# Kernel tuning notes

Hardware: AMD Instinct MI355X
Metric: run time of the kernel (lower is better)

Reference implementation:

```python
import jax, jax.numpy as jnp
import numpy as np

TEMPERATURE = 0.5   # cfg.LOSS.TEMPERATURE
REG = 0.5           # Sinkhorn entropic regularization
NUM_ITER = 100      # numItermax in forward call
STOP_THR = 1e-9

BS, NUM_CLASSES, DIM = 16384, 1000, 512


def _l2norm(x):
    return x / jnp.linalg.norm(x, axis=-1, keepdims=True)


def setup_inputs() -> dict:
    key = jax.random.key(0)
    k1, k2, k3 = jax.random.split(key, 3)
    features = _l2norm(jax.random.normal(k1, (BS, DIM), jnp.float32))
    text_features = _l2norm(jax.random.normal(k2, (NUM_CLASSES, DIM), jnp.float32))
    ratios = jax.random.uniform(k3, (NUM_CLASSES,), jnp.float32)
    ratios = ratios / ratios.sum()  # class prior, sums to 1
    return {"features": features, "text_features": text_features, "ratios": ratios}


def sinkhorn_knopp(a, b, M, reg):
    """Faithful Sinkhorn-Knopp: u/v scaling loop with NaN/Inf bail-out and
    every-10-iters convergence check, unrolled as a masked lax.scan."""
    dim_a, dim_b = a.shape[0], b.shape[0]
    K = jnp.exp(M / -reg)                 # [dim_a, dim_b]
    Kp = (1.0 / a)[:, None] * K           # [dim_a, dim_b]
    u0 = jnp.ones((dim_a,), M.dtype) / dim_a
    v0 = jnp.ones((dim_b,), M.dtype) / dim_b

    def step(carry, ii):
        u, v, done = carry
        KtU = K.T @ u                     # [dim_b]
        v_new = b / KtU
        u_new = 1.0 / (Kp @ v_new)        # [dim_a]
        bad = (jnp.any(KtU == 0)
               | jnp.any(~jnp.isfinite(u_new))
               | jnp.any(~jnp.isfinite(v_new)))
        # err check (original does it when ii % 10 == 0)
        tmp2 = (u_new @ K) * v_new        # einsum('i,ij,j->j', u, K, v)
        err = jnp.linalg.norm(tmp2 - b)
        converged = ((ii % 10) == 0) & (err < STOP_THR)
        keep_prev = done | bad            # revert to uprev/vprev on bad, freeze after done
        u2 = jnp.where(keep_prev, u, u_new)
        v2 = jnp.where(keep_prev, v, v_new)
        return (u2, v2, done | bad | converged), None

    (u, v, _), _ = jax.lax.scan(step, (u0, v0, jnp.array(False)), jnp.arange(NUM_ITER))
    return u[:, None] * K * v[None, :]


def reference(features, text_features, ratios):
    sim_matrix = (features @ text_features.T) / TEMPERATURE   # [bs, C]
    cost_matrix = 1.0 - sim_matrix
    bs = features.shape[0]
    a = jnp.ones((bs,), features.dtype)       # row marginal (uniform over batch)
    b = ratios * bs                            # column marginal (class ratios)
    plan = sinkhorn_knopp(a, b, sim_matrix / cost_matrix, REG)  # [bs, C]
    return plan
```

## Files before the change

### kernel.cpp

```cpp
#include <hip/hip_runtime.h>
#include <hip/hip_bf16.h>

typedef float   f32x4_t  __attribute__((ext_vector_type(4)));
typedef float   f32x2_t  __attribute__((ext_vector_type(2)));
typedef __bf16  bf16x8_t __attribute__((ext_vector_type(8)));
typedef int     i32x4_t  __attribute__((ext_vector_type(4)));

#define N_ROWS   16384
#define N_COLS   1000
#define N_COLS_P 1024
#define N_DIM    512
#define N_ITER   100
#define PBLK     256
#define PTHR     512
#define NRED     64

__device__ __forceinline__ int ldi_sc1(const int* p) {
    return __hip_atomic_load(p, __ATOMIC_RELAXED, __HIP_MEMORY_SCOPE_AGENT);
}
__device__ __forceinline__ void addi_sc1(int* p) {
    __hip_atomic_fetch_add(p, 1, __ATOMIC_RELAXED, __HIP_MEMORY_SCOPE_AGENT);
}
__device__ __forceinline__ f32x2_t ld2_coh(const float* p) {
    f32x2_t v;
    asm volatile("global_load_dwordx2 %0, %1, off sc0 sc1\n\t"
                 "s_waitcnt vmcnt(0)"
                 : "=&v"(v) : "v"(p) : "memory");
    return v;
}
__device__ __forceinline__ void ld4x2_coh(const float* pA, const float* pB,
                                          f32x4_t* a, f32x4_t* b) {
    asm volatile("global_load_dwordx4 %0, %2, off sc0 sc1\n\t"
                 "global_load_dwordx4 %1, %3, off sc0 sc1\n\t"
                 "s_waitcnt vmcnt(0)"
                 : "=&v"(*a), "=&v"(*b) : "v"(pA), "v"(pB) : "memory");
}
__device__ __forceinline__ void st2_coh(float* p, f32x2_t v) {
    asm volatile("global_store_dwordx2 %0, %1, off sc0 sc1"
                 :: "v"(p), "v"(v) : "memory");
}
__device__ __forceinline__ void st1_coh(float* p, float v) {
    asm volatile("global_store_dword %0, %1, off sc0 sc1"
                 :: "v"(p), "v"(v) : "memory");
}
__device__ __forceinline__ void drain_vmem() {
    asm volatile("s_waitcnt vmcnt(0)" ::: "memory");
}

__device__ __forceinline__ unsigned short f2bf(float f) {
    unsigned int u = __builtin_bit_cast(unsigned int, f);
    u += 0x7FFFu + ((u >> 16) & 1u);
    return (unsigned short)(u >> 16);
}

template <int MODE>
__launch_bounds__(256)
__global__ void k_gemm(const float* __restrict__ F, const float* __restrict__ T,
                       void* __restrict__ Kout, float* __restrict__ cpart,
                       const float* __restrict__ v_com, const float* __restrict__ u_both,
                       const int* __restrict__ flags)
{
    __shared__ unsigned short lA[128 * 72];
    __shared__ unsigned short lB[128 * 72];
    __shared__ float cs_lds[4 * 64];

    const int bm = blockIdx.x;
    const int bn = blockIdx.y;
    const int m0 = bm << 7;
    const int n0 = bn << 7;
    const int t  = threadIdx.x;
    const int lane = t & 63;
    const int wid  = t >> 6;
    const int wr = wid >> 1;
    const int wc = wid & 1;

    f32x4_t acc[4][4];
#pragma unroll
    for (int a = 0; a < 4; ++a)
#pragma unroll
        for (int b = 0; b < 4; ++b)
            acc[a][b] = (f32x4_t){0.f, 0.f, 0.f, 0.f};

    const int srow = t >> 4;
    const int scol = (t & 15) << 2;

    for (int kt = 0; kt < N_DIM; kt += 64) {
#pragma unroll
        for (int r = 0; r < 8; ++r) {
            const int rr = srow + (r << 4);
            const float4 av = *(const float4*)(F + (size_t)(m0 + rr) * N_DIM + kt + scol);
            ushort4 a4; a4.x = f2bf(av.x); a4.y = f2bf(av.y); a4.z = f2bf(av.z); a4.w = f2bf(av.w);
            *(ushort4*)(&lA[rr * 72 + scol]) = a4;
            const int gn = n0 + rr;
            float4 bv = make_float4(0.f, 0.f, 0.f, 0.f);
            if (gn < N_COLS) bv = *(const float4*)(T + (size_t)gn * N_DIM + kt + scol);
            ushort4 b4; b4.x = f2bf(bv.x); b4.y = f2bf(bv.y); b4.z = f2bf(bv.z); b4.w = f2bf(bv.w);
            *(ushort4*)(&lB[rr * 72 + scol]) = b4;
        }
        __syncthreads();
#pragma unroll
        for (int ks = 0; ks < 2; ++ks) {
            bf16x8_t afr[4], bfr[4];
#pragma unroll
            for (int mf = 0; mf < 4; ++mf) {
                const int r = (wr << 6) + (mf << 4) + (lane & 15);
                const int off = r * 72 + (ks << 5) + ((lane >> 4) << 3);
                afr[mf] = __builtin_bit_cast(bf16x8_t, *(const i32x4_t*)(&lA[off]));
            }
#pragma unroll
            for (int nf = 0; nf < 4; ++nf) {
                const int r = (wc << 6) + (nf << 4) + (lane & 15);
                const int off = r * 72 + (ks << 5) + ((lane >> 4) << 3);
                bfr[nf] = __builtin_bit_cast(bf16x8_t, *(const i32x4_t*)(&lB[off]));
            }
#pragma unroll
            for (int mf = 0; mf < 4; ++mf)
#pragma unroll
                for (int nf = 0; nf < 4; ++nf)
                    acc[mf][nf] = __builtin_amdgcn_mfma_f32_16x16x32_bf16(
                        afr[mf], bfr[nf], acc[mf][nf], 0, 0, 0);
        }
        __syncthreads();
    }

    int usel = 2;
    if (MODE == 1) usel = flags[1];
    float csum[4] = {0.f, 0.f, 0.f, 0.f};
#pragma unroll
    for (int mf = 0; mf < 4; ++mf) {
#pragma unroll
        for (int nf = 0; nf < 4; ++nf) {
#pragma unroll
            for (int j = 0; j < 4; ++j) {
                const float d = acc[mf][nf][j];
                const float s = 2.f * d;
                const float M = s / (1.f - s);
                const float kv = __expf(-2.f * M);
                const int grow = m0 + (wr << 6) + (mf << 4) + ((lane >> 4) << 2) + j;
                const int gcol = n0 + (wc << 6) + (nf << 4) + (lane & 15);
                if (MODE == 0) {
                    ((unsigned short*)Kout)[(size_t)grow * N_COLS_P + gcol] =
                        (gcol < N_COLS) ? f2bf(kv) : (unsigned short)0;
                    csum[nf] += kv;
                } else {
                    if (gcol < N_COLS) {
                        const float u = (usel == 2) ? (1.f / 16384.f)
                                                    : u_both[(size_t)usel * N_ROWS + grow];
                        ((float*)Kout)[(size_t)grow * N_COLS + gcol] = u * kv * v_com[gcol];
                    }
                }
            }
        }
    }
    if (MODE == 0) {
#pragma unroll
        for (int nf = 0; nf < 4; ++nf) {
            csum[nf] += __shfl_xor(csum[nf], 16);
            csum[nf] += __shfl_xor(csum[nf], 32);
        }
        if (lane < 16) {
#pragma unroll
            for (int nf = 0; nf < 4; ++nf)
                cs_lds[wid * 64 + (nf << 4) + lane] = csum[nf];
        }
        __syncthreads();
        if (t < 128) {
            const int cw = t >> 6;
            const int c6 = t & 63;
            cpart[(size_t)bm * N_COLS_P + n0 + t] =
                cs_lds[cw * 64 + c6] + cs_lds[(cw + 2) * 64 + c6];
        }
    }
}

__launch_bounds__(128)
__global__ void k_init(const float* __restrict__ cpart, float* __restrict__ ktu0,
                       float* __restrict__ vcom, int* __restrict__ flags,
                       int* __restrict__ pcnt, int* __restrict__ rcnt,
                       int* __restrict__ flags2)
{
    const int j = blockIdx.x * 128 + threadIdx.x;
    if (j < N_COLS) {
        float s = 0.f;
        for (int p = 0; p < 128; ++p) s += cpart[(size_t)p * N_COLS_P + j];
        ktu0[j] = s * (1.f / 16384.f);
        vcom[j] = 1.f / 1000.f;
    } else {
        ktu0[j] = 1.f;
        vcom[j] = 0.f;
    }
    for (int z = j; z < 2048; z += 1024) { pcnt[z] = 0; rcnt[z] = 0; flags2[z] = 0; }
    if (j < 4) flags[j] = (j == 1) ? 2 : 0;
}

__launch_bounds__(PTHR, 2)
__global__ void k_persist(const unsigned short* __restrict__ Kb,
                          const float* __restrict__ ratios,
                          float* __restrict__ ktu,
                          float* __restrict__ utmp,
                          float* __restrict__ vcom,
                          float* __restrict__ partials,
                          int* __restrict__ flags,
                          int* __restrict__ pcnt,
                          int* __restrict__ rcnt,
                          int* __restrict__ flags2)
{
    __shared__ float vbuf[2][N_COLS_P];
    __shared__ float wp[8][N_COLS_P];
    __shared__ float redw[8][16];
    __shared__ float rbc;
    __shared__ int ibc;
    const int t = threadIdx.x, lane = t & 63, wid = t >> 6, b = blockIdx.x;
    const int row0 = (b << 6) + (wid << 3);
    const int c2 = t << 1;
    const bool isred = (b < NRED);

    unsigned kp[8][8];
#pragma unroll
    for (int r = 0; r < 8; ++r) {
        const unsigned* rp = (const unsigned*)(Kb + (size_t)(row0 + r) * N_COLS_P);
#pragma unroll
        for (int q = 0; q < 8; ++q) kp[r][q] = rp[(q << 6) + lane];
    }
    const float bj0 = (c2 < N_COLS) ? ratios[c2] * 16384.f : 0.f;
    const float bj1 = (c2 + 1 < N_COLS) ? ratios[c2 + 1] * 16384.f : 0.f;

    int usel = 2;

    for (int ii = 0; ii <= N_ITER; ++ii) {
        const int p = ii & 1;
        f32x2_t kc;

        if (ii > 0) {
            if (t == 0) {
                while (ldi_sc1(&rcnt[(ii - 1) << 4]) < NRED)
                    __builtin_amdgcn_s_sleep(1);
                ibc = ldi_sc1(&flags2[(ii - 1) << 4]);
            }
            __syncthreads();
            if (ibc) break;
            usel = (ii - 1) & 1;
            kc = ld2_coh(&ktu[(p << 10) + c2]);
            if (((ii - 1) % 10) == 0) {
                const float vo0 = vbuf[usel][c2], vo1 = vbuf[usel][c2 + 1];
                const float d0 = (c2 < N_COLS) ? kc[0] * vo0 - bj0 : 0.f;
                const float d1 = (c2 + 1 < N_COLS) ? kc[1] * vo1 - bj1 : 0.f;
                float e = d0 * d0 + d1 * d1;
#pragma unroll
                for (int sh = 1; sh <= 32; sh <<= 1) e += __shfl_xor(e, sh);
                if (lane == 0) redw[wid][0] = e;
                __syncthreads();
                if (t == 0) {
                    float s = 0.f;
#pragma unroll
                    for (int w = 0; w < 8; ++w) s += redw[w][0];
                    rbc = s;
                }
                __syncthreads();
                if (rbc < 1e-18f) break;
            }
            if (ii == N_ITER) break;
        } else {
            kc = ld2_coh(&ktu[c2]);
        }

        const float v0 = bj0 / kc[0];
        const float v1 = bj1 / kc[1];
        const int badv = (kc[0] == 0.f) | (kc[1] == 0.f) |
                         (!isfinite(v0)) | (!isfinite(v1));
        *(f32x2_t*)&vbuf[p][c2] = (f32x2_t){v0, v1};
        if (__syncthreads_or(badv)) break;

        float vr[16];
#pragma unroll
        for (int q = 0; q < 8; ++q) {
            const f32x2_t vv = *(const f32x2_t*)&vbuf[p][(q << 7) + (lane << 1)];
            vr[2*q] = vv[0]; vr[2*q+1] = vv[1];
        }
        float dots[8];
#pragma unroll
        for (int r = 0; r < 8; ++r) {
            float p0 = 0.f, p1 = 0.f, p2 = 0.f, p3 = 0.f;
#pragma unroll
            for (int q = 0; q < 8; ++q) {
                const unsigned u = kp[r][q];
                const float lo = __builtin_bit_cast(float, u << 16);
                const float hi = __builtin_bit_cast(float, u & 0xFFFF0000u);
                if (q & 1) { p2 = fmaf(lo, vr[2*q], p2); p3 = fmaf(hi, vr[2*q+1], p3); }
                else       { p0 = fmaf(lo, vr[2*q], p0); p1 = fmaf(hi, vr[2*q+1], p1); }
            }
            dots[r] = (p0 + p1) + (p2 + p3);
        }
#pragma unroll
        for (int s = 1; s <= 32; s <<= 1) {
#pragma unroll
            for (int r = 0; r < 8; ++r) dots[r] += __shfl_xor(dots[r], s);
        }
        float u8[8];
        int ubad = 0;
#pragma unroll
        for (int r = 0; r < 8; ++r) { u8[r] = 1.f / dots[r]; ubad |= !isfinite(u8[r]); }
        if (lane == 0) {
            float* uo = utmp + ((size_t)p << 14) + row0;
#pragma unroll
            for (int r = 0; r < 8; ++r) uo[r] = u8[r];
        }
        if (__any(ubad) && lane == 0)
            __hip_atomic_fetch_or(&flags2[ii << 4], 1, __ATOMIC_RELAXED,
                                  __HIP_MEMORY_SCOPE_AGENT);

        float creg[16];
#pragma unroll
        for (int e = 0; e < 16; ++e) creg[e] = 0.f;
#pragma unroll
        for (int r = 0; r < 8; ++r) {
#pragma unroll
            for (int q = 0; q < 8; ++q) {
                const unsigned u = kp[r][q];
                const float lo = __builtin_bit_cast(float, u << 16);
                const float hi = __builtin_bit_cast(float, u & 0xFFFF0000u);
                creg[2*q]   = fmaf(lo, u8[r], creg[2*q]);
                creg[2*q+1] = fmaf(hi, u8[r], creg[2*q+1]);
            }
        }
#pragma unroll
        for (int q = 0; q < 8; ++q)
            *(f32x2_t*)&wp[wid][(q << 7) + (lane << 1)] = (f32x2_t){creg[2*q], creg[2*q+1]};
        __syncthreads();
        {
            const int j2 = t << 1;
            f32x2_t s2 = *(const f32x2_t*)&wp[0][j2];
#pragma unroll
            for (int w = 1; w < 8; ++w) {
                const f32x2_t x = *(const f32x2_t*)&wp[w][j2];
                s2[0] += x[0]; s2[1] += x[1];
            }
            st2_coh(&partials[((size_t)b << 10) + j2], s2);
        }
        drain_vmem();
        __syncthreads();
        if (t == 0) addi_sc1(&pcnt[ii << 4]);

        if (isred) {
            if (t == 0) {
                while (ldi_sc1(&pcnt[ii << 4]) < PBLK)
                    __builtin_amdgcn_s_sleep(1);
            }
            __syncthreads();
            const int cbase = (b << 4) + ((lane & 3) << 2);
            const int rowA  = (wid << 4) + (lane >> 2);
            f32x4_t a, bq;
            ld4x2_coh(&partials[((size_t)rowA << 10) + cbase],
                      &partials[((size_t)(rowA + 128) << 10) + cbase], &a, &bq);
            f32x4_t s4;
#pragma unroll
            for (int e = 0; e < 4; ++e) s4[e] = a[e] + bq[e];
#pragma unroll
            for (int sh = 4; sh <= 32; sh <<= 1) {
#pragma unroll
                for (int e = 0; e < 4; ++e) s4[e] += __shfl_xor(s4[e], sh);
            }
            if (lane < 4) *(f32x4_t*)&redw[wid][lane << 2] = s4;
            __syncthreads();
            if (t < 16) {
                float s2 = 0.f;
#pragma unroll
                for (int w = 0; w < 8; ++w) s2 += redw[w][t];
                const int c = (b << 4) + t;
                st1_coh(&ktu[(((ii + 1) & 1) << 10) + c], (c < N_COLS) ? s2 : 1.f);
            }
            drain_vmem();
            __syncthreads();
            if (t == 0) addi_sc1(&rcnt[ii << 4]);
        }
    }

    if (b == 0) {
        if (c2 < N_COLS)
            vcom[c2] = (usel == 2) ? (1.f / 1000.f) : vbuf[usel][c2];
        if (c2 + 1 < N_COLS)
            vcom[c2 + 1] = (usel == 2) ? (1.f / 1000.f) : vbuf[usel][c2 + 1];
        if (t == 0) flags[1] = usel;
    }
}

extern "C" void kernel_launch(void* const* d_in, const int* in_sizes, int n_in,
                              void* d_out, int out_size, void* d_ws, size_t ws_size,
                              hipStream_t stream)
{
    const float* F      = (const float*)d_in[0];
    const float* T      = (const float*)d_in[1];
    const float* ratios = (const float*)d_in[2];
    float* out = (float*)d_out;
    unsigned short* Kb = (unsigned short*)d_out;

    float* ws        = (float*)d_ws;
    float* partials  = ws;
    float* ktu       = partials + (size_t)PBLK * N_COLS_P;
    float* utmp      = ktu + 2 * N_COLS_P;
    float* vcom      = utmp + 2 * N_ROWS;
    int*   flags     = (int*)(vcom + N_COLS_P);
    int*   pcnt      = flags + 16;
    int*   rcnt      = pcnt + 2048;
    int*   flags2    = rcnt + 2048;
    const size_t need_bytes = ((size_t)PBLK * N_COLS_P + 2 * N_COLS_P + 2 * N_ROWS +
                               N_COLS_P) * sizeof(float) +
                              (16 + 3 * 2048) * sizeof(int);
    if (ws_size < need_bytes) return;

    k_gemm<0><<<dim3(128, 8), 256, 0, stream>>>(F, T, Kb, partials, nullptr, nullptr, flags);
    k_init<<<8, 128, 0, stream>>>(partials, ktu, vcom, flags, pcnt, rcnt, flags2);
    k_persist<<<PBLK, PTHR, 0, stream>>>(Kb, ratios, ktu, utmp, vcom, partials,
                                         flags, pcnt, rcnt, flags2);
    k_gemm<1><<<dim3(128, 8), 256, 0, stream>>>(F, T, out, nullptr, vcom, utmp, flags);
}
```

Baseline: 2.235 ms.

## Replace two-phase partial reduction with float atomics into per-iteration slots

Each block now atomically adds its per-column partial sums into a per-iteration slot buffer, padded to 16 bytes per column. This removes the dedicated reducer blocks and leaves one global barrier per iteration instead of two, so the write-partials / wait / reduce / wait chain collapses into one atomic accumulation and one counter wait. In exchange it issues 256×1000 float atomics per iteration, which contend on the same addresses, and it adds an init kernel that zeroes 100 slots. It also drops the per-row u non-finite check and only detects bad values through non-finite column sums, and the atomics make the summation order nondeterministic.

```diff
diff --git a/kernel.cpp b/kernel.cpp
--- a/kernel.cpp
+++ b/kernel.cpp
@@ -13,7 +13,7 @@
 #define N_ITER   100
 #define PBLK     256
 #define PTHR     512
-#define NRED     64
+#define SLOTF    4096
 
 __device__ __forceinline__ int ldi_sc1(const int* p) {
     return __hip_atomic_load(p, __ATOMIC_RELAXED, __HIP_MEMORY_SCOPE_AGENT);
@@ -21,27 +21,15 @@
 __device__ __forceinline__ void addi_sc1(int* p) {
     __hip_atomic_fetch_add(p, 1, __ATOMIC_RELAXED, __HIP_MEMORY_SCOPE_AGENT);
 }
-__device__ __forceinline__ f32x2_t ld2_coh(const float* p) {
-    f32x2_t v;
-    asm volatile("global_load_dwordx2 %0, %1, off sc0 sc1\n\t"
+__device__ __forceinline__ void addf_sc1(float* p, float v) {
+    __hip_atomic_fetch_add(p, v, __ATOMIC_RELAXED, __HIP_MEMORY_SCOPE_AGENT);
+}
+__device__ __forceinline__ void ld2x1_coh(const float* p0, const float* p1,
+                                          float* a, float* b) {
+    asm volatile("global_load_dword %0, %2, off sc0 sc1\n\t"
+                 "global_load_dword %1, %3, off sc0 sc1\n\t"
                  "s_waitcnt vmcnt(0)"
-                 : "=&v"(v) : "v"(p) : "memory");
-    return v;
-}
-__device__ __forceinline__ void ld4x2_coh(const float* pA, const float* pB,
-                                          f32x4_t* a, f32x4_t* b) {
-    asm volatile("global_load_dwordx4 %0, %2, off sc0 sc1\n\t"
-                 "global_load_dwordx4 %1, %3, off sc0 sc1\n\t"
-                 "s_waitcnt vmcnt(0)"
-                 : "=&v"(*a), "=&v"(*b) : "v"(pA), "v"(pB) : "memory");
-}
-__device__ __forceinline__ void st2_coh(float* p, f32x2_t v) {
-    asm volatile("global_store_dwordx2 %0, %1, off sc0 sc1"
-                 :: "v"(p), "v"(v) : "memory");
-}
-__device__ __forceinline__ void st1_coh(float* p, float v) {
-    asm volatile("global_store_dword %0, %1, off sc0 sc1"
-                 :: "v"(p), "v"(v) : "memory");
+                 : "=&v"(*a), "=&v"(*b) : "v"(p0), "v"(p1) : "memory");
 }
 __device__ __forceinline__ void drain_vmem() {
     asm volatile("s_waitcnt vmcnt(0)" ::: "memory");
@@ -174,46 +162,51 @@
 }
 
 __launch_bounds__(128)
-__global__ void k_init(const float* __restrict__ cpart, float* __restrict__ ktu0,
-                       float* __restrict__ vcom, int* __restrict__ flags,
-                       int* __restrict__ pcnt, int* __restrict__ rcnt,
-                       int* __restrict__ flags2)
+__global__ void k_init1(const float* __restrict__ cpart, float* __restrict__ ktu0)
 {
     const int j = blockIdx.x * 128 + threadIdx.x;
     if (j < N_COLS) {
         float s = 0.f;
         for (int p = 0; p < 128; ++p) s += cpart[(size_t)p * N_COLS_P + j];
         ktu0[j] = s * (1.f / 16384.f);
-        vcom[j] = 1.f / 1000.f;
     } else {
         ktu0[j] = 1.f;
-        vcom[j] = 0.f;
-    }
-    for (int z = j; z < 2048; z += 1024) { pcnt[z] = 0; rcnt[z] = 0; flags2[z] = 0; }
-    if (j < 4) flags[j] = (j == 1) ? 2 : 0;
+    }
+}
+
+__launch_bounds__(256)
+__global__ void k_init2(float* __restrict__ slots, int* __restrict__ done,
+                        int* __restrict__ flags)
+{
+    const int idx = blockIdx.x * 256 + threadIdx.x;
+    if (idx < N_ITER * 1024) {
+        f32x4_t v = (f32x4_t){0.f, 0.f, 0.f, 0.f};
+        if ((idx & 1023) >= N_COLS) v[0] = 1.f;
+        *(f32x4_t*)&slots[(size_t)idx << 2] = v;
+    }
+    if (blockIdx.x == 0) {
+        for (int z = threadIdx.x; z < N_ITER * 16; z += 256) done[z] = 0;
+        if (threadIdx.x < 16) flags[threadIdx.x] = (threadIdx.x == 1) ? 2 : 0;
+    }
 }
 
 __launch_bounds__(PTHR, 2)
 __global__ void k_persist(const unsigned short* __restrict__ Kb,
                           const float* __restrict__ ratios,
-                          float* __restrict__ ktu,
+                          const float* __restrict__ ktu0,
+                          float* __restrict__ slots,
                           float* __restrict__ utmp,
                           float* __restrict__ vcom,
-                          float* __restrict__ partials,
                           int* __restrict__ flags,
-                          int* __restrict__ pcnt,
-                          int* __restrict__ rcnt,
-                          int* __restrict__ flags2)
+                          int* __restrict__ done)
 {
     __shared__ float vbuf[2][N_COLS_P];
     __shared__ float wp[8][N_COLS_P];
-    __shared__ float redw[8][16];
+    __shared__ float cw[8];
     __shared__ float rbc;
-    __shared__ int ibc;
     const int t = threadIdx.x, lane = t & 63, wid = t >> 6, b = blockIdx.x;
     const int row0 = (b << 6) + (wid << 3);
     const int c2 = t << 1;
-    const bool isred = (b < NRED);
 
     unsigned kp[8][8];
 #pragma unroll
@@ -228,32 +221,33 @@
     int usel = 2;
 
     for (int ii = 0; ii <= N_ITER; ++ii) {
-        const int p = ii & 1;
-        f32x2_t kc;
+        const int sp = ii & 1;
+        float kc0, kc1;
 
         if (ii > 0) {
             if (t == 0) {
-                while (ldi_sc1(&rcnt[(ii - 1) << 4]) < NRED)
+                while (ldi_sc1(&done[(ii - 1) << 4]) < PBLK)
                     __builtin_amdgcn_s_sleep(1);
-                ibc = ldi_sc1(&flags2[(ii - 1) << 4]);
             }
             __syncthreads();
-            if (ibc) break;
+            const float* sl = slots + (size_t)(ii - 1) * SLOTF;
+            ld2x1_coh(sl + (size_t)c2 * 4, sl + (size_t)c2 * 4 + 4, &kc0, &kc1);
+            const int badk = (!isfinite(kc0)) | (!isfinite(kc1));
+            if (__syncthreads_or(badk)) break;
             usel = (ii - 1) & 1;
-            kc = ld2_coh(&ktu[(p << 10) + c2]);
             if (((ii - 1) % 10) == 0) {
                 const float vo0 = vbuf[usel][c2], vo1 = vbuf[usel][c2 + 1];
-                const float d0 = (c2 < N_COLS) ? kc[0] * vo0 - bj0 : 0.f;
-                const float d1 = (c2 + 1 < N_COLS) ? kc[1] * vo1 - bj1 : 0.f;
+                const float d0 = (c2 < N_COLS) ? kc0 * vo0 - bj0 : 0.f;
+                const float d1 = (c2 + 1 < N_COLS) ? kc1 * vo1 - bj1 : 0.f;
                 float e = d0 * d0 + d1 * d1;
 #pragma unroll
                 for (int sh = 1; sh <= 32; sh <<= 1) e += __shfl_xor(e, sh);
-                if (lane == 0) redw[wid][0] = e;
+                if (lane == 0) cw[wid] = e;
                 __syncthreads();
                 if (t == 0) {
                     float s = 0.f;
 #pragma unroll
-                    for (int w = 0; w < 8; ++w) s += redw[w][0];
+                    for (int w = 0; w < 8; ++w) s += cw[w];
                     rbc = s;
                 }
                 __syncthreads();
@@ -261,20 +255,21 @@
             }
             if (ii == N_ITER) break;
         } else {
-            kc = ld2_coh(&ktu[c2]);
-        }
-
-        const float v0 = bj0 / kc[0];
-        const float v1 = bj1 / kc[1];
-        const int badv = (kc[0] == 0.f) | (kc[1] == 0.f) |
+            kc0 = ktu0[c2];
+            kc1 = ktu0[c2 + 1];
+        }
+
+        const float v0 = bj0 / kc0;
+        const float v1 = bj1 / kc1;
+        const int badv = (kc0 == 0.f) | (kc1 == 0.f) |
                          (!isfinite(v0)) | (!isfinite(v1));
-        *(f32x2_t*)&vbuf[p][c2] = (f32x2_t){v0, v1};
+        vbuf[sp][c2] = v0; vbuf[sp][c2 + 1] = v1;
         if (__syncthreads_or(badv)) break;
 
         float vr[16];
 #pragma unroll
         for (int q = 0; q < 8; ++q) {
-            const f32x2_t vv = *(const f32x2_t*)&vbuf[p][(q << 7) + (lane << 1)];
+            const f32x2_t vv = *(const f32x2_t*)&vbuf[sp][(q << 7) + (lane << 1)];
             vr[2*q] = vv[0]; vr[2*q+1] = vv[1];
         }
         float dots[8];
@@ -297,17 +292,13 @@
             for (int r = 0; r < 8; ++r) dots[r] += __shfl_xor(dots[r], s);
         }
         float u8[8];
-        int ubad = 0;
-#pragma unroll
-        for (int r = 0; r < 8; ++r) { u8[r] = 1.f / dots[r]; ubad |= !isfinite(u8[r]); }
+#pragma unroll
+        for (int r = 0; r < 8; ++r) u8[r] = 1.f / dots[r];
         if (lane == 0) {
-            float* uo = utmp + ((size_t)p << 14) + row0;
+            float* uo = utmp + ((size_t)sp << 14) + row0;
 #pragma unroll
             for (int r = 0; r < 8; ++r) uo[r] = u8[r];
         }
-        if (__any(ubad) && lane == 0)
-            __hip_atomic_fetch_or(&flags2[ii << 4], 1, __ATOMIC_RELAXED,
-                                  __HIP_MEMORY_SCOPE_AGENT);
 
         float creg[16];
 #pragma unroll
@@ -335,44 +326,13 @@
                 const f32x2_t x = *(const f32x2_t*)&wp[w][j2];
                 s2[0] += x[0]; s2[1] += x[1];
             }
-            st2_coh(&partials[((size_t)b << 10) + j2], s2);
+            float* sl = slots + (size_t)ii * SLOTF;
+            if (j2 < N_COLS)     addf_sc1(sl + (size_t)j2 * 4, s2[0]);
+            if (j2 + 1 < N_COLS) addf_sc1(sl + (size_t)(j2 + 1) * 4, s2[1]);
         }
         drain_vmem();
         __syncthreads();
-        if (t == 0) addi_sc1(&pcnt[ii << 4]);
-
-        if (isred) {
-            if (t == 0) {
-                while (ldi_sc1(&pcnt[ii << 4]) < PBLK)
-                    __builtin_amdgcn_s_sleep(1);
-            }
-            __syncthreads();
-            const int cbase = (b << 4) + ((lane & 3) << 2);
-            const int rowA  = (wid << 4) + (lane >> 2);
-            f32x4_t a, bq;
-            ld4x2_coh(&partials[((size_t)rowA << 10) + cbase],
-                      &partials[((size_t)(rowA + 128) << 10) + cbase], &a, &bq);
-            f32x4_t s4;
-#pragma unroll
-            for (int e = 0; e < 4; ++e) s4[e] = a[e] + bq[e];
-#pragma unroll
-            for (int sh = 4; sh <= 32; sh <<= 1) {
-#pragma unroll
-                for (int e = 0; e < 4; ++e) s4[e] += __shfl_xor(s4[e], sh);
-            }
-            if (lane < 4) *(f32x4_t*)&redw[wid][lane << 2] = s4;
-            __syncthreads();
-            if (t < 16) {
-                float s2 = 0.f;
-#pragma unroll
-                for (int w = 0; w < 8; ++w) s2 += redw[w][t];
-                const int c = (b << 4) + t;
-                st1_coh(&ktu[(((ii + 1) & 1) << 10) + c], (c < N_COLS) ? s2 : 1.f);
-            }
-            drain_vmem();
-            __syncthreads();
-            if (t == 0) addi_sc1(&rcnt[ii << 4]);
-        }
+        if (t == 0) addi_sc1(&done[ii << 4]);
     }
 
     if (b == 0) {
@@ -395,22 +355,22 @@
     unsigned short* Kb = (unsigned short*)d_out;
 
     float* ws        = (float*)d_ws;
-    float* partials  = ws;
-    float* ktu       = partials + (size_t)PBLK * N_COLS_P;
-    float* utmp      = ktu + 2 * N_COLS_P;
+    float* slots     = ws;
+    float* cpart     = slots;
+    float* ktu0      = slots + (size_t)N_ITER * SLOTF;
+    float* utmp      = ktu0 + N_COLS_P;
     float* vcom      = utmp + 2 * N_ROWS;
     int*   flags     = (int*)(vcom + N_COLS_P);
-    int*   pcnt      = flags + 16;
-    int*   rcnt      = pcnt + 2048;
-    int*   flags2    = rcnt + 2048;
-    const size_t need_bytes = ((size_t)PBLK * N_COLS_P + 2 * N_COLS_P + 2 * N_ROWS +
+    int*   done      = flags + 16;
+    const size_t need_bytes = ((size_t)N_ITER * SLOTF + N_COLS_P + 2 * N_ROWS +
                                N_COLS_P) * sizeof(float) +
-                              (16 + 3 * 2048) * sizeof(int);
+                              (16 + N_ITER * 16) * sizeof(int);
     if (ws_size < need_bytes) return;
 
-    k_gemm<0><<<dim3(128, 8), 256, 0, stream>>>(F, T, Kb, partials, nullptr, nullptr, flags);
-    k_init<<<8, 128, 0, stream>>>(partials, ktu, vcom, flags, pcnt, rcnt, flags2);
-    k_persist<<<PBLK, PTHR, 0, stream>>>(Kb, ratios, ktu, utmp, vcom, partials,
-                                         flags, pcnt, rcnt, flags2);
+    k_gemm<0><<<dim3(128, 8), 256, 0, stream>>>(F, T, Kb, cpart, nullptr, nullptr, flags);
+    k_init1<<<8, 128, 0, stream>>>(cpart, ktu0);
+    k_init2<<<400, 256, 0, stream>>>(slots, done, flags);
+    k_persist<<<PBLK, PTHR, 0, stream>>>(Kb, ratios, ktu0, slots, utmp, vcom,
+                                         flags, done);
     k_gemm<1><<<dim3(128, 8), 256, 0, stream>>>(F, T, out, nullptr, vcom, utmp, flags);
 }
```

After: 3.134 ms. 40.2% more time.
